# Optimization experiments

Measured on AMD Instinct MI355X. Metric: run time of the kernel, lower is better.

The kernel has to match this reference:

```python
import jax, jax.numpy as jnp
import numpy as np

ITERATIONS = 3
OUT_CAPS, OUT_DIM = 10, 16


def squash(x):
    # square_norm / (1 + square_norm) * x / (sqrt(square_norm) + 1e-6), norm over last axis
    sn = jnp.sum(x * x, axis=-1, keepdims=True)
    return sn / (1.0 + sn) * x / (jnp.sqrt(sn) + 1e-6)


def setup_inputs() -> dict:
    key = jax.random.key(0)
    kx, kw = jax.random.split(key)
    x = jax.random.normal(kx, (256, 32, 6, 6, 8), dtype=jnp.float32)
    W = 0.01 * jax.random.normal(kw, (1, 32, 6, 6, 10, 8, 16), dtype=jnp.float32)
    return {"x": x, "W": W}


def reference(x, W):
    w = W[0]  # [i,j,k,o,d,e]
    # u_hat: prediction vectors, [B, i, j, k, O, E]
    u_hat = jnp.einsum('bijkd,ijkode->bijkoe', x, w)
    u_det = jax.lax.stop_gradient(u_hat)
    b = jnp.zeros(u_hat.shape[:-1], dtype=u_hat.dtype)  # [B,i,j,k,O]
    for _ in range(ITERATIONS - 1):
        c = jax.nn.softmax(b, axis=-1)
        s = jnp.einsum('bijko,bijkoe->boe', c, u_det)   # reduce over all input-capsule axes
        v = squash(s)                                    # [B,O,E]
        b = b + jnp.einsum('bijkoe,boe->bijko', u_det, v)
    c = jax.nn.softmax(b, axis=-1)
    s = jnp.einsum('bijko,bijkoe->boe', c, u_hat)
    v = squash(s)
    return v.reshape(-1, OUT_CAPS, OUT_DIM)
```

## Files before the change

kernel.cpp:

```cpp
#include <hip/hip_runtime.h>
#include <math.h>

#define BATCH 256
#define IC    1152
#define DD    8
#define OO    10
#define EE    16
#define BTILE 64
#define NBT   4
#define NT    640
#define CHUNK 8
#define NCHUNK 144
#define WPC   (OO * DD * EE)

__global__ __launch_bounds__(NT) void caps_pass_kernel(
    const float* __restrict__ x,
    const float* __restrict__ W,
    const float* __restrict__ V,
    float* __restrict__ s_part,
    int first)
{
    __shared__ float w_lds[CHUNK][WPC];
    __shared__ float x_lds[CHUNK][DD][BTILE];
    __shared__ float elg_lds[2][NT];

    const int tid = threadIdx.x;
    const int o   = tid >> 6;
    const int bl  = tid & 63;
    const int b   = blockIdx.y * BTILE + bl;
    const int ijk0 = blockIdx.x * CHUNK;

    {
        const float4* wg = reinterpret_cast<const float4*>(W + (size_t)ijk0 * WPC);
        float4* wl = reinterpret_cast<float4*>(&w_lds[0][0]);
        #pragma unroll
        for (int i = 0; i < (CHUNK * WPC / 4) / NT; ++i)
            wl[tid + i * NT] = wg[tid + i * NT];
    }

    {
        const float* xgrp = x + (size_t)(blockIdx.y * BTILE) * (IC * DD);
        #pragma unroll 1
        for (int i = tid; i < CHUNK * BTILE * 2; i += NT) {
            const int lq = i & 1;
            const int lb = (i >> 1) & 63;
            const int ls = i >> 7;
            const float4 t = *reinterpret_cast<const float4*>(
                xgrp + (size_t)lb * (IC * DD) + (size_t)(ijk0 + ls) * DD + lq * 4);
            x_lds[ls][lq * 4 + 0][lb] = t.x;
            x_lds[ls][lq * 4 + 1][lb] = t.y;
            x_lds[ls][lq * 4 + 2][lb] = t.z;
            x_lds[ls][lq * 4 + 3][lb] = t.w;
        }
    }

    float vreg[EE];
    if (!first) {
        const float4* vp = reinterpret_cast<const float4*>(V + ((size_t)b * OO + o) * EE);
        #pragma unroll
        for (int q = 0; q < 4; ++q) {
            float4 t = vp[q];
            vreg[q * 4 + 0] = t.x; vreg[q * 4 + 1] = t.y;
            vreg[q * 4 + 2] = t.z; vreg[q * 4 + 3] = t.w;
        }
    }
    __syncthreads();

    float sacc[EE];
    #pragma unroll
    for (int e = 0; e < EE; ++e) sacc[e] = 0.f;

    int p = 0;
    #pragma unroll 1
    for (int s = 0; s < CHUNK; ++s) {
        const float4* wq = reinterpret_cast<const float4*>(&w_lds[s][o * (DD * EE)]);

        float u[EE];
        #pragma unroll
        for (int e = 0; e < EE; ++e) u[e] = 0.f;
        #pragma unroll
        for (int d = 0; d < DD; ++d) {
            const float xv = x_lds[s][d][bl];
            #pragma unroll
            for (int q = 0; q < 4; ++q) {
                const float4 w4 = wq[d * 4 + q];
                u[q * 4 + 0] = fmaf(xv, w4.x, u[q * 4 + 0]);
                u[q * 4 + 1] = fmaf(xv, w4.y, u[q * 4 + 1]);
                u[q * 4 + 2] = fmaf(xv, w4.z, u[q * 4 + 2]);
                u[q * 4 + 3] = fmaf(xv, w4.w, u[q * 4 + 3]);
            }
        }

        float c;
        if (!first) {
            float lg = 0.f;
            #pragma unroll
            for (int e = 0; e < EE; ++e) lg = fmaf(u[e], vreg[e], lg);
            const float elg = __expf(lg);
            elg_lds[p][tid] = elg;
            __syncthreads();
            float den = 0.f;
            #pragma unroll
            for (int oo = 0; oo < OO; ++oo)
                den += elg_lds[p][oo * 64 + bl];
            c = __fdividef(elg, den);
            p ^= 1;
        } else {
            c = 1.0f;
        }

        #pragma unroll
        for (int e = 0; e < EE; ++e)
            sacc[e] = fmaf(c, u[e], sacc[e]);
    }

    const float mul = first ? 0.1f : 1.0f;
    float* sp = s_part + (((size_t)blockIdx.x * BATCH + b) * OO + o) * EE;
    #pragma unroll
    for (int q = 0; q < 4; ++q) {
        float4 t;
        t.x = mul * sacc[q * 4 + 0]; t.y = mul * sacc[q * 4 + 1];
        t.z = mul * sacc[q * 4 + 2]; t.w = mul * sacc[q * 4 + 3];
        reinterpret_cast<float4*>(sp)[q] = t;
    }
}

__global__ __launch_bounds__(256) void caps_squash_kernel(
    const float* __restrict__ s_part,
    float* __restrict__ V,
    float* __restrict__ out,
    int accum, int last)
{
    __shared__ float red[3][64];
    const int lane = threadIdx.x & 63;
    const int w    = threadIdx.x >> 6;
    const int g    = blockIdx.x * 64 + lane;

    const float* sp = s_part + g;
    float s = 0.f;
    #pragma unroll 4
    for (int ch = w * (NCHUNK / 4); ch < (w + 1) * (NCHUNK / 4); ++ch)
        s += sp[(size_t)ch * (BATCH * OO * EE)];

    if (w > 0) red[w - 1][lane] = s;
    __syncthreads();
    if (w == 0) {
        s += red[0][lane] + red[1][lane] + red[2][lane];

        float sq = s * s;
        #pragma unroll
        for (int m = 1; m < 16; m <<= 1) sq += __shfl_xor(sq, m, 16);

        float scale = sq / (1.f + sq) / (sqrtf(sq) + 1e-6f);
        float v = scale * s;

        if (last)       out[g] = v;
        else if (accum) V[g]  += v;
        else            V[g]   = v;
    }
}

extern "C" void kernel_launch(void* const* d_in, const int* in_sizes, int n_in,
                              void* d_out, int out_size, void* d_ws, size_t ws_size,
                              hipStream_t stream) {
    const float* x = (const float*)d_in[0];
    const float* W = (const float*)d_in[1];
    float* out = (float*)d_out;

    float* s_part = (float*)d_ws;
    float* V      = s_part + (size_t)NCHUNK * BATCH * OO * EE;

    dim3 grid(NCHUNK, NBT), blk(NT);
    const int sq_blocks = (BATCH * OO * EE) / 64;

    caps_pass_kernel<<<grid, blk, 0, stream>>>(x, W, V, s_part, 1);
    caps_squash_kernel<<<sq_blocks, 256, 0, stream>>>(s_part, V, out, 0, 0);
    caps_pass_kernel<<<grid, blk, 0, stream>>>(x, W, V, s_part, 0);
    caps_squash_kernel<<<sq_blocks, 256, 0, stream>>>(s_part, V, out, 1, 0);
    caps_pass_kernel<<<grid, blk, 0, stream>>>(x, W, V, s_part, 0);
    caps_squash_kernel<<<sq_blocks, 256, 0, stream>>>(s_part, V, out, 0, 1);
}
```

Measured before the change: 184.8 us.

## Compute u_hat with bf16x3 split MFMA and in-register softmax over capsules

Replaces the scalar FP32 FMA computation of prediction vectors with MFMA 16x16x32 bf16 instructions. Each fp32 operand is split into hi/lo bf16 parts, and the K dimension packs the hi*hi, lo*hi and hi*lo products to keep near-fp32 accuracy. The block shrinks to 256 threads, with each wave holding all 10 output capsules for 16 batch rows. This lets the routing softmax run in registers with lane shuffles instead of an LDS exchange and barrier on every step. Output partial sums are staged through LDS for coalesced stores, at the cost of extra conversion work and some precision risk.

```diff
diff --git a/kernel.cpp b/kernel.cpp
--- a/kernel.cpp
+++ b/kernel.cpp
@@ -8,10 +8,21 @@
 #define EE    16
 #define BTILE 64
 #define NBT   4
-#define NT    640
+#define NT    256
 #define CHUNK 8
 #define NCHUNK 144
-#define WPC   (OO * DD * EE)
+
+typedef __attribute__((ext_vector_type(8))) short short8;
+typedef __attribute__((ext_vector_type(4))) float f32x4;
+
+__device__ __forceinline__ unsigned short f2bf(float f) {
+    unsigned u = __float_as_uint(f);
+    unsigned r = u + 0x7FFFu + ((u >> 16) & 1u);
+    return (unsigned short)(r >> 16);
+}
+__device__ __forceinline__ float bf2f(unsigned short h) {
+    return __uint_as_float(((unsigned)h) << 16);
+}
 
 __global__ __launch_bounds__(NT) void caps_pass_kernel(
     const float* __restrict__ x,
@@ -20,108 +31,142 @@
     float* __restrict__ s_part,
     int first)
 {
-    __shared__ float w_lds[CHUNK][WPC];
-    __shared__ float x_lds[CHUNK][DD][BTILE];
-    __shared__ float elg_lds[2][NT];
-
-    const int tid = threadIdx.x;
-    const int o   = tid >> 6;
-    const int bl  = tid & 63;
-    const int b   = blockIdx.y * BTILE + bl;
+    __shared__ __align__(16) char smem[57360];
+    unsigned short* w_hi = (unsigned short*)(smem);
+    unsigned short* w_lo = (unsigned short*)(smem + 20480);
+    unsigned short* x_hi = (unsigned short*)(smem + 40960);
+    unsigned short* x_lo = (unsigned short*)(smem + 49152);
+    unsigned short* zpad = (unsigned short*)(smem + 57344);
+
+    const int tid  = threadIdx.x;
+    const int wv   = tid >> 6;
+    const int lane = tid & 63;
+    const int q    = lane >> 4;
+    const int em   = lane & 15;
     const int ijk0 = blockIdx.x * CHUNK;
-
-    {
-        const float4* wg = reinterpret_cast<const float4*>(W + (size_t)ijk0 * WPC);
-        float4* wl = reinterpret_cast<float4*>(&w_lds[0][0]);
-        #pragma unroll
-        for (int i = 0; i < (CHUNK * WPC / 4) / NT; ++i)
-            wl[tid + i * NT] = wg[tid + i * NT];
-    }
-
-    {
-        const float* xgrp = x + (size_t)(blockIdx.y * BTILE) * (IC * DD);
-        #pragma unroll 1
-        for (int i = tid; i < CHUNK * BTILE * 2; i += NT) {
-            const int lq = i & 1;
-            const int lb = (i >> 1) & 63;
-            const int ls = i >> 7;
+    const int bg0  = blockIdx.y * BTILE;
+
+    if (tid < 4) ((unsigned*)zpad)[tid] = 0u;
+
+    {
+        const float4* wg4 = reinterpret_cast<const float4*>(W + (size_t)ijk0 * (OO*DD*EE));
+        #pragma unroll
+        for (int i = 0; i < 10; ++i) {
+            const int f = tid + i * NT;
+            const float4 t = wg4[f];
+            const int l4 = f << 2;
+            const int e0 = l4 & 15;
+            int rr = l4 >> 4;
+            const int d = rr & 7; rr >>= 3;
+            const int o = rr % 10, s = rr / 10;
+            const float vv[4] = {t.x, t.y, t.z, t.w};
+            #pragma unroll
+            for (int j = 0; j < 4; ++j) {
+                const unsigned short h = f2bf(vv[j]);
+                const unsigned short l = f2bf(vv[j] - bf2f(h));
+                const int off = (s*160 + o*16 + e0 + j) * 8 + d;
+                w_hi[off] = h; w_lo[off] = l;
+            }
+        }
+    }
+    {
+        #pragma unroll
+        for (int i = 0; i < 2; ++i) {
+            const int u = tid + i * NT;
+            const int b = u >> 3, s = u & 7;
+            const float* xp = x + ((size_t)(bg0 + b) * IC + (ijk0 + s)) * DD;
+            const float4 xa = *reinterpret_cast<const float4*>(xp);
+            const float4 xb = *reinterpret_cast<const float4*>(xp + 4);
+            const float vv[8] = {xa.x,xa.y,xa.z,xa.w, xb.x,xb.y,xb.z,xb.w};
+            short8 hv, lv;
+            #pragma unroll
+            for (int j = 0; j < 8; ++j) {
+                const unsigned short h = f2bf(vv[j]);
+                hv[j] = (short)h;
+                lv[j] = (short)f2bf(vv[j] - bf2f(h));
+            }
+            const int off = (s*64 + b) * 8;
+            *reinterpret_cast<short8*>(&x_hi[off]) = hv;
+            *reinterpret_cast<short8*>(&x_lo[off]) = lv;
+        }
+    }
+
+    f32x4 vreg[OO];
+    if (!first) {
+        const int bgl = bg0 + 16*wv + em;
+        #pragma unroll
+        for (int o = 0; o < OO; ++o) {
             const float4 t = *reinterpret_cast<const float4*>(
-                xgrp + (size_t)lb * (IC * DD) + (size_t)(ijk0 + ls) * DD + lq * 4);
-            x_lds[ls][lq * 4 + 0][lb] = t.x;
-            x_lds[ls][lq * 4 + 1][lb] = t.y;
-            x_lds[ls][lq * 4 + 2][lb] = t.z;
-            x_lds[ls][lq * 4 + 3][lb] = t.w;
-        }
-    }
-
-    float vreg[EE];
-    if (!first) {
-        const float4* vp = reinterpret_cast<const float4*>(V + ((size_t)b * OO + o) * EE);
-        #pragma unroll
-        for (int q = 0; q < 4; ++q) {
-            float4 t = vp[q];
-            vreg[q * 4 + 0] = t.x; vreg[q * 4 + 1] = t.y;
-            vreg[q * 4 + 2] = t.z; vreg[q * 4 + 3] = t.w;
-        }
-    }
-    __syncthreads();
-
-    float sacc[EE];
+                V + (size_t)bgl * (OO*EE) + o*EE + 4*q);
+            vreg[o] = (f32x4){t.x, t.y, t.z, t.w};
+        }
+    }
+
+    __syncthreads();
+
+    const unsigned short* wbase = (q==1) ? w_lo : ((q==3) ? zpad : w_hi);
+    const unsigned short* xbase = (q==2) ? x_lo : ((q==3) ? zpad : x_hi);
+    const int msk = (q==3) ? 0 : 1;
+
+    f32x4 sacc[OO];
     #pragma unroll
-    for (int e = 0; e < EE; ++e) sacc[e] = 0.f;
-
-    int p = 0;
+    for (int o = 0; o < OO; ++o) sacc[o] = (f32x4){0.f,0.f,0.f,0.f};
+
     #pragma unroll 1
     for (int s = 0; s < CHUNK; ++s) {
-        const float4* wq = reinterpret_cast<const float4*>(&w_lds[s][o * (DD * EE)]);
-
-        float u[EE];
-        #pragma unroll
-        for (int e = 0; e < EE; ++e) u[e] = 0.f;
-        #pragma unroll
-        for (int d = 0; d < DD; ++d) {
-            const float xv = x_lds[s][d][bl];
-            #pragma unroll
-            for (int q = 0; q < 4; ++q) {
-                const float4 w4 = wq[d * 4 + q];
-                u[q * 4 + 0] = fmaf(xv, w4.x, u[q * 4 + 0]);
-                u[q * 4 + 1] = fmaf(xv, w4.y, u[q * 4 + 1]);
-                u[q * 4 + 2] = fmaf(xv, w4.z, u[q * 4 + 2]);
-                u[q * 4 + 3] = fmaf(xv, w4.w, u[q * 4 + 3]);
+        const short8 xf = *reinterpret_cast<const short8*>(
+            xbase + msk * ((s*64 + 16*wv + em) * 8));
+        f32x4 u[OO];
+        #pragma unroll
+        for (int o = 0; o < OO; ++o) {
+            const short8 wf = *reinterpret_cast<const short8*>(
+                wbase + msk * ((s*160 + o*16 + em) * 8));
+            u[o] = __builtin_amdgcn_mfma_f32_16x16x32_bf16(
+                       wf, xf, (f32x4){0.f,0.f,0.f,0.f}, 0, 0, 0);
+        }
+        if (!first) {
+            float elg[OO];
+            float den = 0.f;
+            #pragma unroll
+            for (int o = 0; o < OO; ++o) {
+                float t = u[o][0]*vreg[o][0] + u[o][1]*vreg[o][1]
+                        + u[o][2]*vreg[o][2] + u[o][3]*vreg[o][3];
+                t += __shfl_xor(t, 16);
+                t += __shfl_xor(t, 32);
+                elg[o] = __expf(t);
+                den += elg[o];
             }
-        }
-
-        float c;
-        if (!first) {
-            float lg = 0.f;
-            #pragma unroll
-            for (int e = 0; e < EE; ++e) lg = fmaf(u[e], vreg[e], lg);
-            const float elg = __expf(lg);
-            elg_lds[p][tid] = elg;
-            __syncthreads();
-            float den = 0.f;
-            #pragma unroll
-            for (int oo = 0; oo < OO; ++oo)
-                den += elg_lds[p][oo * 64 + bl];
-            c = __fdividef(elg, den);
-            p ^= 1;
+            const float rden = __fdividef(1.0f, den);
+            #pragma unroll
+            for (int o = 0; o < OO; ++o)
+                sacc[o] += u[o] * (elg[o] * rden);
         } else {
-            c = 1.0f;
-        }
-
-        #pragma unroll
-        for (int e = 0; e < EE; ++e)
-            sacc[e] = fmaf(c, u[e], sacc[e]);
-    }
-
+            #pragma unroll
+            for (int o = 0; o < OO; ++o) sacc[o] += u[o];
+        }
+    }
+
+    __syncthreads();
+    float* sout = (float*)smem;
     const float mul = first ? 0.1f : 1.0f;
-    float* sp = s_part + (((size_t)blockIdx.x * BATCH + b) * OO + o) * EE;
-    #pragma unroll
-    for (int q = 0; q < 4; ++q) {
-        float4 t;
-        t.x = mul * sacc[q * 4 + 0]; t.y = mul * sacc[q * 4 + 1];
-        t.z = mul * sacc[q * 4 + 2]; t.w = mul * sacc[q * 4 + 3];
-        reinterpret_cast<float4*>(sp)[q] = t;
+    {
+        const int bl = 16*wv + em;
+        #pragma unroll
+        for (int o = 0; o < OO; ++o)
+            #pragma unroll
+            for (int r = 0; r < 4; ++r)
+                sout[bl*168 + o*16 + 4*q + r] = mul * sacc[o][r];
+    }
+    __syncthreads();
+    {
+        float* sp = s_part + ((size_t)blockIdx.x * BATCH + bg0) * (OO*EE);
+        #pragma unroll
+        for (int i = 0; i < 10; ++i) {
+            const int f = tid + i*NT;
+            const int b = f / 40, c4 = (f % 40) * 4;
+            const float4 t = *reinterpret_cast<const float4*>(&sout[b*168 + c4]);
+            *reinterpret_cast<float4*>(&sp[(size_t)b*(OO*EE) + c4]) = t;
+        }
     }
 }
 
```

New measurement: 150.7 us. -18.4%, faster.
